# Kernel tuning notes

Measured on AMD Instinct MI355X. Metric: run time of the kernel, lower is better.

Reference implementation:

```python
import jax, jax.numpy as jnp
import numpy as np

B, N, M = 8, 131072, 64
M_VALID = 48  # trailing padding, matches remove_pad semantics
POSITIVE_IOU = 0.5
NEGATIVE_IOU = 0.3
CLASS_NUM = 1  # hardcoded in RpnTarget.__init__


def _make_boxes(key, shape_prefix, max_wh=64.0, span=1024.0):
    k1, k2, k3, k4 = jax.random.split(key, 4)
    x1 = jax.random.uniform(k1, shape_prefix, minval=0.0, maxval=span)
    y1 = jax.random.uniform(k2, shape_prefix, minval=0.0, maxval=span)
    w = jax.random.uniform(k3, shape_prefix, minval=4.0, maxval=max_wh)
    h = jax.random.uniform(k4, shape_prefix, minval=4.0, maxval=max_wh)
    return jnp.stack([x1, y1, x1 + w, y1 + h], axis=-1)


def setup_inputs() -> dict:
    key = jax.random.key(0)
    ka, kb = jax.random.split(key, 2)
    prior_anchors = _make_boxes(ka, (B, N))                       # [B,N,4]
    boxes = _make_boxes(kb, (B, M), max_wh=128.0)                 # [B,M,4]
    status = jnp.concatenate(
        [jnp.ones((B, M_VALID, 1)), jnp.zeros((B, M - M_VALID, 1))], axis=1
    )
    gt_bboxes = jnp.concatenate([boxes, status], axis=-1)          # [B,M,5]
    gt_class_idxes = jnp.zeros((B, M, 2), dtype=jnp.int32)         # zeroed in call()
    return {
        "prior_anchors": prior_anchors,
        "gt_bboxes": gt_bboxes,
        "gt_class_idxes": gt_class_idxes,
    }


def _bbox_transform(anchors, bboxes):
    # anchors, bboxes: [..., 4] in [x1,y1,x2,y2]
    ax = (anchors[..., 0] + anchors[..., 2]) * 0.5
    ay = (anchors[..., 1] + anchors[..., 3]) * 0.5
    aw = anchors[..., 2] - anchors[..., 0]
    ah = anchors[..., 3] - anchors[..., 1]
    bx = (bboxes[..., 0] + bboxes[..., 2]) * 0.5
    by = (bboxes[..., 1] + bboxes[..., 3]) * 0.5
    bw = bboxes[..., 2] - bboxes[..., 0]
    bh = bboxes[..., 3] - bboxes[..., 1]
    tx = (bx - ax) / aw
    ty = (by - ay) / ah
    tw = jnp.log(bw / aw)
    th = jnp.log(bh / ah)
    return jnp.stack([tx, ty, tw, th], axis=-1)


def _rpn_targets(prior_anchors, gt_bboxes, gt_class_idxes):
    boxes = gt_bboxes[..., :4]                 # [B,M,4]
    valid = gt_bboxes[..., 4] > 0              # [B,M] padding status

    a = prior_anchors[:, :, None, :]           # [B,N,1,4]
    b = boxes[:, None, :, :]                   # [B,1,M,4]
    inter_w = jnp.maximum(jnp.minimum(a[..., 2], b[..., 2]) - jnp.maximum(a[..., 0], b[..., 0]), 0.0)
    inter_h = jnp.maximum(jnp.minimum(a[..., 3], b[..., 3]) - jnp.maximum(a[..., 1], b[..., 1]), 0.0)
    inter = inter_w * inter_h                  # [B,N,M]
    area_a = jnp.maximum(a[..., 2] - a[..., 0], 0.0) * jnp.maximum(a[..., 3] - a[..., 1], 0.0)
    area_b = jnp.maximum(b[..., 2] - b[..., 0], 0.0) * jnp.maximum(b[..., 3] - b[..., 1], 0.0)
    iou = inter / (area_a + area_b - inter)    # [B,N,M]
    # mask out padded gt boxes (equivalent to remove_pad + trailing padding)
    iou = jnp.where(valid[:, None, :], iou, -1.0)

    max_iou = jnp.max(iou, axis=-1)            # [B,N]
    match_idx = jnp.argmax(iou, axis=-1)       # [B,N]
    positive = max_iou >= POSITIVE_IOU
    ignore = (max_iou >= NEGATIVE_IOU) & ~positive

    matched_boxes = jnp.take_along_axis(boxes, match_idx[..., None], axis=1)  # [B,N,4]
    reg = _bbox_transform(prior_anchors, matched_boxes)                        # [B,N,4]

    status = jnp.where(positive, 1.0, jnp.where(ignore, -1.0, 0.0))[..., None]  # [B,N,1]

    # call() zeros gt_class_idxes, so matched class idx is always 0; one_hot depth 1 -> ones
    cls_idx = jnp.take_along_axis(
        jnp.zeros_like(gt_class_idxes)[..., 0], match_idx, axis=1
    )                                                                           # [B,N] int32 zeros
    cls = jax.nn.one_hot(cls_idx, CLASS_NUM, dtype=reg.dtype)                   # [B,N,1]

    regression_targets = jnp.concatenate([reg, status], axis=-1)                # [B,N,5]
    classification_targets = jnp.concatenate([cls, status], axis=-1)            # [B,N,2]
    return regression_targets, classification_targets


def reference(prior_anchors, gt_bboxes, gt_class_idxes):
    return _rpn_targets(prior_anchors, gt_bboxes, gt_class_idxes)
```

## Files before the change

kernel.cpp:

```cpp
#include <hip/hip_runtime.h>


#define BB    8
#define NN    131072
#define MM    64
#define BLK   256
#define NBLK  (NN / BLK)
#define GC    16
#define CELLS (GC * GC)
#define CAP   32

#define WS_BOXES 0
#define WS_AREA  8192
#define WS_CNT   10240
#define WS_LIST  10272
#define WS_LEN   75808

typedef float  f4v __attribute__((ext_vector_type(4)));
typedef float  f2v __attribute__((ext_vector_type(2)));
typedef unsigned long long u64;
typedef unsigned char u8;

__global__ __launch_bounds__(256) void rpn_build_lists(
    const float* __restrict__ gt, char* __restrict__ ws)
{
    __shared__ float4 sbox[MM];
    __shared__ int    scnt;

    const int b = blockIdx.x;
    const int t = threadIdx.x;

    float4* wboxes = (float4*)(ws + WS_BOXES);
    float*  warea  = (float*)(ws + WS_AREA);
    int*    wcnt   = (int*)(ws + WS_CNT);
    u8*     wlist  = (u8*)(ws + WS_LIST);
    u8*     wlen   = (u8*)(ws + WS_LEN);

    if (t < MM) {
        const float* g = gt + ((size_t)b * MM + t) * 5;
        float x1 = g[0], y1 = g[1], x2 = g[2], y2 = g[3], st = g[4];
        bool valid = (st > 0.0f);
        u64 mask = __ballot(valid);
        int slot = __popcll(mask & ((1ull << t) - 1ull));
        int cntL = __popcll(mask);
        if (t == 0) { scnt = cntL; wcnt[b] = cntL; }
        if (valid) {
            float4 bx = make_float4(x1, y1, x2, y2);
            sbox[slot] = bx;
            wboxes[b * MM + slot] = bx;
            warea[b * MM + slot]  = fmaxf(x2 - x1, 0.0f) * fmaxf(y2 - y1, 0.0f);
        }
        if (t >= cntL) {
            wboxes[b * MM + t] = make_float4(0.f, 0.f, 0.f, 0.f);
            warea[b * MM + t]  = 0.f;
        }
    }
    __syncthreads();

    const int cnt = scnt;
    const int cx = t & (GC - 1), cy = t >> 4;
    const float wx1 = cx * 64.0f, wx2 = wx1 + 128.0f;
    const float wy1 = cy * 64.0f, wy2 = wy1 + 128.0f;

    u64* lq = (u64*)(wlist + ((size_t)b * CELLS + t) * CAP);
    lq[0] = ~0ull; lq[1] = ~0ull; lq[2] = ~0ull; lq[3] = ~0ull;
    u8* lst = (u8*)lq;

    int len = 0;
    for (int s = 0; s < cnt; ++s) {
        float4 bx = sbox[s];
        if (bx.x <= wx2 && bx.z >= wx1 && bx.y <= wy2 && bx.w >= wy1) {
            if (len < CAP) lst[len] = (u8)s;
            ++len;
        }
    }
    wlen[(size_t)b * CELLS + t] = (u8)len;
}

__global__ __launch_bounds__(BLK) void rpn_target_kernel(
    const float* __restrict__ anchors,
    const float* __restrict__ gt,
    const char* __restrict__ ws,
    float* __restrict__ out)
{
    constexpr float INV = GC / 1024.0f;

    __shared__ float sx1[MM], sy1[MM], sx2[MM], sy2[MM], sar[MM];
    __shared__ int   scnt;

    const int t = threadIdx.x;
    const int b = blockIdx.x / NBLK;
    const int n = (blockIdx.x % NBLK) * BLK + t;

    const f4v av = __builtin_nontemporal_load(
        (const f4v*)anchors + (size_t)b * NN + n);
    const float4 a = make_float4(av.x, av.y, av.z, av.w);

    if (t < MM) {
        float4 bx = ((const float4*)(ws + WS_BOXES))[b * MM + t];
        sx1[t] = bx.x; sy1[t] = bx.y; sx2[t] = bx.z; sy2[t] = bx.w;
        sar[t] = ((const float*)(ws + WS_AREA))[b * MM + t];
    }
    if (t == 0) scnt = ((const int*)(ws + WS_CNT))[b];

    int cx = (int)(a.x * INV); cx = cx < 0 ? 0 : (cx > GC - 1 ? GC - 1 : cx);
    int cy = (int)(a.y * INV); cy = cy < 0 ? 0 : (cy > GC - 1 ? GC - 1 : cy);
    const int cid = cy * GC + cx;

    const u64 lst8 = *(const u64*)(ws + WS_LIST + ((size_t)b * CELLS + cid) * CAP);
    const int len  = ((const u8*)(ws + WS_LEN))[(size_t)b * CELLS + cid];

    const float area_a = fmaxf(a.z - a.x, 0.0f) * fmaxf(a.w - a.y, 0.0f);

    __syncthreads();
    const int cnt = scnt;

    float best  = 0.0f;
    int   bslot = 0;

    float iou[8]; int id[8];
    #pragma unroll
    for (int j = 0; j < 8; ++j) {
        const int raw = (int)((lst8 >> (8 * j)) & 0xFFull);
        const int idx = raw & 63;
        id[j] = idx;
        const float bx1 = sx1[idx], by1 = sy1[idx];
        const float bx2 = sx2[idx], by2 = sy2[idx];
        float iw = fmaxf(fminf(a.z, bx2) - fmaxf(a.x, bx1), 0.0f);
        float ih = fmaxf(fminf(a.w, by2) - fmaxf(a.y, by1), 0.0f);
        float inter = iw * ih;
        inter = (raw != 255) ? inter : 0.0f;
        float denom = (area_a + sar[idx]) - inter;
        iou[j] = inter / denom;
    }
    #pragma unroll
    for (int j = 0; j < 8; ++j)
        if (iou[j] > best) { best = iou[j]; bslot = id[j]; }

    if (__any(len > 8)) {
        const u8* gl = (const u8*)(ws + WS_LIST + ((size_t)b * CELLS + cid) * CAP);
        const int L = (len <= CAP) ? len : 0;
        for (int j = 8; j < L; ++j) {
            const int idx = gl[j];
            float iw = fmaxf(fminf(a.z, sx2[idx]) - fmaxf(a.x, sx1[idx]), 0.0f);
            float ih = fmaxf(fminf(a.w, sy2[idx]) - fmaxf(a.y, sy1[idx]), 0.0f);
            float inter = iw * ih;
            if (inter > 0.0f) {
                float denom = (area_a + sar[idx]) - inter;
                float iou2 = inter / denom;
                if (iou2 > best) { best = iou2; bslot = idx; }
            }
        }
    }
    if (__any(len > CAP)) {
        if (len > CAP) {
            best = 0.0f; bslot = 0;
            for (int j = 0; j < cnt; ++j) {
                float iw = fmaxf(fminf(a.z, sx2[j]) - fmaxf(a.x, sx1[j]), 0.0f);
                float ih = fmaxf(fminf(a.w, sy2[j]) - fmaxf(a.y, sy1[j]), 0.0f);
                float inter = iw * ih;
                if (inter > 0.0f) {
                    float denom = (area_a + sar[j]) - inter;
                    float iou2 = inter / denom;
                    if (iou2 > best) { best = iou2; bslot = j; }
                }
            }
        }
    }

    const float status = (best >= 0.5f) ? 1.0f : ((best >= 0.3f) ? -1.0f : 0.0f);

    float mx1, my1, mx2, my2;
    if (cnt > 0) {
        mx1 = sx1[bslot]; my1 = sy1[bslot]; mx2 = sx2[bslot]; my2 = sy2[bslot];
    } else {
        const float* g0 = gt + (size_t)b * MM * 5;
        mx1 = g0[0]; my1 = g0[1]; mx2 = g0[2]; my2 = g0[3];
    }

    const float aw  = a.z - a.x;
    const float ah  = a.w - a.y;
    const float rw  = __builtin_amdgcn_rcpf(aw);
    const float rh  = __builtin_amdgcn_rcpf(ah);
    const float tx  = ((mx1 + mx2) * 0.5f - (a.x + a.z) * 0.5f) * rw;
    const float ty  = ((my1 + my2) * 0.5f - (a.y + a.w) * 0.5f) * rh;
    const float LN2 = 0.69314718055994531f;
    const float tw  = __builtin_amdgcn_logf((mx2 - mx1) * rw) * LN2;
    const float th  = __builtin_amdgcn_logf((my2 - my1) * rh) * LN2;

    const size_t gid = (size_t)b * NN + n;

    float* r = out + gid * 5;
    __builtin_nontemporal_store(tx,     &r[0]);
    __builtin_nontemporal_store(ty,     &r[1]);
    __builtin_nontemporal_store(tw,     &r[2]);
    __builtin_nontemporal_store(th,     &r[3]);
    __builtin_nontemporal_store(status, &r[4]);

    f2v cv; cv.x = 1.0f; cv.y = status;
    __builtin_nontemporal_store(cv, (f2v*)(out + (size_t)BB * NN * 5) + gid);
}

extern "C" void kernel_launch(void* const* d_in, const int* in_sizes, int n_in,
                              void* d_out, int out_size, void* d_ws, size_t ws_size,
                              hipStream_t stream) {
    const float* anchors = (const float*)d_in[0];
    const float* gt      = (const float*)d_in[1];

    float* out = (float*)d_out;
    char*  ws  = (char*)d_ws;

    hipLaunchKernelGGL(rpn_build_lists, dim3(BB), dim3(256), 0, stream, gt, ws);
    hipLaunchKernelGGL(rpn_target_kernel, dim3(BB * NBLK), dim3(BLK), 0, stream,
                       anchors, gt, ws, out);
}
```

Baseline: 25.60 us.

## Fuse list build and target kernels into one cooperative persistent kernel

Merges the grid-cell list construction and the per-anchor IoU/target kernel into a single cooperative launch. A grid-wide sync separates the two phases, and a persistent grid of 1024 blocks loops over the 4096 anchor slices. Nontemporal loads and stores are also replaced with ordinary ones. This removes one kernel launch and the gap between the two kernels, at the cost of grid-sync overhead, cooperative launch overhead, and reloading shared box data on every slice iteration.

```diff
diff --git a/kernel.cpp b/kernel.cpp
--- a/kernel.cpp
+++ b/kernel.cpp
@@ -1,4 +1,5 @@
 #include <hip/hip_runtime.h>
+#include <hip/hip_cooperative_groups.h>
 
 
 #define BB    8
@@ -6,6 +7,8 @@
 #define MM    64
 #define BLK   256
 #define NBLK  (NN / BLK)
+#define NSLICE (BB * NBLK)
+#define GRID  1024
 #define GC    16
 #define CELLS (GC * GC)
 #define CAP   32
@@ -16,189 +19,185 @@
 #define WS_LIST  10272
 #define WS_LEN   75808
 
-typedef float  f4v __attribute__((ext_vector_type(4)));
-typedef float  f2v __attribute__((ext_vector_type(2)));
 typedef unsigned long long u64;
 typedef unsigned char u8;
 
-__global__ __launch_bounds__(256) void rpn_build_lists(
-    const float* __restrict__ gt, char* __restrict__ ws)
-{
-    __shared__ float4 sbox[MM];
-    __shared__ int    scnt;
-
-    const int b = blockIdx.x;
-    const int t = threadIdx.x;
-
-    float4* wboxes = (float4*)(ws + WS_BOXES);
-    float*  warea  = (float*)(ws + WS_AREA);
-    int*    wcnt   = (int*)(ws + WS_CNT);
-    u8*     wlist  = (u8*)(ws + WS_LIST);
-    u8*     wlen   = (u8*)(ws + WS_LEN);
-
-    if (t < MM) {
-        const float* g = gt + ((size_t)b * MM + t) * 5;
-        float x1 = g[0], y1 = g[1], x2 = g[2], y2 = g[3], st = g[4];
-        bool valid = (st > 0.0f);
-        u64 mask = __ballot(valid);
-        int slot = __popcll(mask & ((1ull << t) - 1ull));
-        int cntL = __popcll(mask);
-        if (t == 0) { scnt = cntL; wcnt[b] = cntL; }
-        if (valid) {
-            float4 bx = make_float4(x1, y1, x2, y2);
-            sbox[slot] = bx;
-            wboxes[b * MM + slot] = bx;
-            warea[b * MM + slot]  = fmaxf(x2 - x1, 0.0f) * fmaxf(y2 - y1, 0.0f);
-        }
-        if (t >= cntL) {
-            wboxes[b * MM + t] = make_float4(0.f, 0.f, 0.f, 0.f);
-            warea[b * MM + t]  = 0.f;
-        }
-    }
-    __syncthreads();
-
-    const int cnt = scnt;
-    const int cx = t & (GC - 1), cy = t >> 4;
-    const float wx1 = cx * 64.0f, wx2 = wx1 + 128.0f;
-    const float wy1 = cy * 64.0f, wy2 = wy1 + 128.0f;
-
-    u64* lq = (u64*)(wlist + ((size_t)b * CELLS + t) * CAP);
-    lq[0] = ~0ull; lq[1] = ~0ull; lq[2] = ~0ull; lq[3] = ~0ull;
-    u8* lst = (u8*)lq;
-
-    int len = 0;
-    for (int s = 0; s < cnt; ++s) {
-        float4 bx = sbox[s];
-        if (bx.x <= wx2 && bx.z >= wx1 && bx.y <= wy2 && bx.w >= wy1) {
-            if (len < CAP) lst[len] = (u8)s;
-            ++len;
-        }
-    }
-    wlen[(size_t)b * CELLS + t] = (u8)len;
-}
-
-__global__ __launch_bounds__(BLK) void rpn_target_kernel(
+namespace cg = cooperative_groups;
+
+__global__ __launch_bounds__(BLK) void rpn_fused(
     const float* __restrict__ anchors,
     const float* __restrict__ gt,
-    const char* __restrict__ ws,
+    char* __restrict__ ws,
     float* __restrict__ out)
 {
     constexpr float INV = GC / 1024.0f;
 
-    __shared__ float sx1[MM], sy1[MM], sx2[MM], sy2[MM], sar[MM];
-    __shared__ int   scnt;
+    __shared__ float4 sbox[MM];
+    __shared__ float  sx1[MM], sy1[MM], sx2[MM], sy2[MM], sar[MM];
+    __shared__ int    scnt;
 
     const int t = threadIdx.x;
-    const int b = blockIdx.x / NBLK;
-    const int n = (blockIdx.x % NBLK) * BLK + t;
-
-    const f4v av = __builtin_nontemporal_load(
-        (const f4v*)anchors + (size_t)b * NN + n);
-    const float4 a = make_float4(av.x, av.y, av.z, av.w);
-
-    if (t < MM) {
-        float4 bx = ((const float4*)(ws + WS_BOXES))[b * MM + t];
-        sx1[t] = bx.x; sy1[t] = bx.y; sx2[t] = bx.z; sy2[t] = bx.w;
-        sar[t] = ((const float*)(ws + WS_AREA))[b * MM + t];
+
+    if (blockIdx.x < BB) {
+        const int b = blockIdx.x;
+
+        float4* wboxes = (float4*)(ws + WS_BOXES);
+        float*  warea  = (float*)(ws + WS_AREA);
+        int*    wcnt   = (int*)(ws + WS_CNT);
+        u8*     wlist  = (u8*)(ws + WS_LIST);
+        u8*     wlen   = (u8*)(ws + WS_LEN);
+
+        if (t < MM) {
+            const float* g = gt + ((size_t)b * MM + t) * 5;
+            float x1 = g[0], y1 = g[1], x2 = g[2], y2 = g[3], st = g[4];
+            bool valid = (st > 0.0f);
+            u64 mask = __ballot(valid);
+            int slot = __popcll(mask & ((1ull << t) - 1ull));
+            int cntL = __popcll(mask);
+            if (t == 0) { scnt = cntL; wcnt[b] = cntL; }
+            if (valid) {
+                float4 bx = make_float4(x1, y1, x2, y2);
+                sbox[slot] = bx;
+                wboxes[b * MM + slot] = bx;
+                warea[b * MM + slot]  = fmaxf(x2 - x1, 0.0f) * fmaxf(y2 - y1, 0.0f);
+            }
+            if (t >= cntL) {
+                wboxes[b * MM + t] = make_float4(0.f, 0.f, 0.f, 0.f);
+                warea[b * MM + t]  = 0.f;
+            }
+        }
+        __syncthreads();
+
+        const int cnt = scnt;
+        const int cx = t & (GC - 1), cy = t >> 4;
+        const float wx1 = cx * 64.0f, wx2 = wx1 + 128.0f;
+        const float wy1 = cy * 64.0f, wy2 = wy1 + 128.0f;
+
+        u64* lq = (u64*)(wlist + ((size_t)b * CELLS + t) * CAP);
+        lq[0] = ~0ull; lq[1] = ~0ull; lq[2] = ~0ull; lq[3] = ~0ull;
+        u8* lst = (u8*)lq;
+
+        int len = 0;
+        for (int s = 0; s < cnt; ++s) {
+            float4 bx = sbox[s];
+            if (bx.x <= wx2 && bx.z >= wx1 && bx.y <= wy2 && bx.w >= wy1) {
+                if (len < CAP) lst[len] = (u8)s;
+                ++len;
+            }
+        }
+        wlen[(size_t)b * CELLS + t] = (u8)len;
+        __threadfence();
     }
-    if (t == 0) scnt = ((const int*)(ws + WS_CNT))[b];
-
-    int cx = (int)(a.x * INV); cx = cx < 0 ? 0 : (cx > GC - 1 ? GC - 1 : cx);
-    int cy = (int)(a.y * INV); cy = cy < 0 ? 0 : (cy > GC - 1 ? GC - 1 : cy);
-    const int cid = cy * GC + cx;
-
-    const u64 lst8 = *(const u64*)(ws + WS_LIST + ((size_t)b * CELLS + cid) * CAP);
-    const int len  = ((const u8*)(ws + WS_LEN))[(size_t)b * CELLS + cid];
-
-    const float area_a = fmaxf(a.z - a.x, 0.0f) * fmaxf(a.w - a.y, 0.0f);
-
-    __syncthreads();
-    const int cnt = scnt;
-
-    float best  = 0.0f;
-    int   bslot = 0;
-
-    float iou[8]; int id[8];
-    #pragma unroll
-    for (int j = 0; j < 8; ++j) {
-        const int raw = (int)((lst8 >> (8 * j)) & 0xFFull);
-        const int idx = raw & 63;
-        id[j] = idx;
-        const float bx1 = sx1[idx], by1 = sy1[idx];
-        const float bx2 = sx2[idx], by2 = sy2[idx];
-        float iw = fmaxf(fminf(a.z, bx2) - fmaxf(a.x, bx1), 0.0f);
-        float ih = fmaxf(fminf(a.w, by2) - fmaxf(a.y, by1), 0.0f);
-        float inter = iw * ih;
-        inter = (raw != 255) ? inter : 0.0f;
-        float denom = (area_a + sar[idx]) - inter;
-        iou[j] = inter / denom;
-    }
-    #pragma unroll
-    for (int j = 0; j < 8; ++j)
-        if (iou[j] > best) { best = iou[j]; bslot = id[j]; }
-
-    if (__any(len > 8)) {
-        const u8* gl = (const u8*)(ws + WS_LIST + ((size_t)b * CELLS + cid) * CAP);
-        const int L = (len <= CAP) ? len : 0;
-        for (int j = 8; j < L; ++j) {
-            const int idx = gl[j];
-            float iw = fmaxf(fminf(a.z, sx2[idx]) - fmaxf(a.x, sx1[idx]), 0.0f);
-            float ih = fmaxf(fminf(a.w, sy2[idx]) - fmaxf(a.y, sy1[idx]), 0.0f);
+
+    cg::this_grid().sync();
+
+    for (int s = blockIdx.x; s < NSLICE; s += GRID) {
+        const int b = s / NBLK;
+        const int n = (s % NBLK) * BLK + t;
+
+        const float4 a = ((const float4*)anchors)[(size_t)b * NN + n];
+
+        __syncthreads();
+        if (t < MM) {
+            float4 bx = ((const float4*)(ws + WS_BOXES))[b * MM + t];
+            sx1[t] = bx.x; sy1[t] = bx.y; sx2[t] = bx.z; sy2[t] = bx.w;
+            sar[t] = ((const float*)(ws + WS_AREA))[b * MM + t];
+        }
+        if (t == 0) scnt = ((const int*)(ws + WS_CNT))[b];
+
+        int cx = (int)(a.x * INV); cx = cx < 0 ? 0 : (cx > GC - 1 ? GC - 1 : cx);
+        int cy = (int)(a.y * INV); cy = cy < 0 ? 0 : (cy > GC - 1 ? GC - 1 : cy);
+        const int cid = cy * GC + cx;
+
+        const u64 lst8 = *(const u64*)(ws + WS_LIST + ((size_t)b * CELLS + cid) * CAP);
+        const int len  = ((const u8*)(ws + WS_LEN))[(size_t)b * CELLS + cid];
+
+        const float area_a = fmaxf(a.z - a.x, 0.0f) * fmaxf(a.w - a.y, 0.0f);
+
+        __syncthreads();
+        const int cnt = scnt;
+
+        float best  = 0.0f;
+        int   bslot = 0;
+
+        float iou[8]; int id[8];
+        #pragma unroll
+        for (int j = 0; j < 8; ++j) {
+            const int raw = (int)((lst8 >> (8 * j)) & 0xFFull);
+            const int idx = raw & 63;
+            id[j] = idx;
+            const float bx1 = sx1[idx], by1 = sy1[idx];
+            const float bx2 = sx2[idx], by2 = sy2[idx];
+            float iw = fmaxf(fminf(a.z, bx2) - fmaxf(a.x, bx1), 0.0f);
+            float ih = fmaxf(fminf(a.w, by2) - fmaxf(a.y, by1), 0.0f);
             float inter = iw * ih;
-            if (inter > 0.0f) {
-                float denom = (area_a + sar[idx]) - inter;
-                float iou2 = inter / denom;
-                if (iou2 > best) { best = iou2; bslot = idx; }
-            }
-        }
-    }
-    if (__any(len > CAP)) {
-        if (len > CAP) {
-            best = 0.0f; bslot = 0;
-            for (int j = 0; j < cnt; ++j) {
-                float iw = fmaxf(fminf(a.z, sx2[j]) - fmaxf(a.x, sx1[j]), 0.0f);
-                float ih = fmaxf(fminf(a.w, sy2[j]) - fmaxf(a.y, sy1[j]), 0.0f);
+            inter = (raw != 255) ? inter : 0.0f;
+            float denom = (area_a + sar[idx]) - inter;
+            iou[j] = inter / denom;
+        }
+        #pragma unroll
+        for (int j = 0; j < 8; ++j)
+            if (iou[j] > best) { best = iou[j]; bslot = id[j]; }
+
+        if (__any(len > 8)) {
+            const u8* gl = (const u8*)(ws + WS_LIST + ((size_t)b * CELLS + cid) * CAP);
+            const int L = (len <= CAP) ? len : 0;
+            for (int j = 8; j < L; ++j) {
+                const int idx = gl[j];
+                float iw = fmaxf(fminf(a.z, sx2[idx]) - fmaxf(a.x, sx1[idx]), 0.0f);
+                float ih = fmaxf(fminf(a.w, sy2[idx]) - fmaxf(a.y, sy1[idx]), 0.0f);
                 float inter = iw * ih;
                 if (inter > 0.0f) {
-                    float denom = (area_a + sar[j]) - inter;
+                    float denom = (area_a + sar[idx]) - inter;
                     float iou2 = inter / denom;
-                    if (iou2 > best) { best = iou2; bslot = j; }
+                    if (iou2 > best) { best = iou2; bslot = idx; }
                 }
             }
         }
+        if (__any(len > CAP)) {
+            if (len > CAP) {
+                best = 0.0f; bslot = 0;
+                for (int j = 0; j < cnt; ++j) {
+                    float iw = fmaxf(fminf(a.z, sx2[j]) - fmaxf(a.x, sx1[j]), 0.0f);
+                    float ih = fmaxf(fminf(a.w, sy2[j]) - fmaxf(a.y, sy1[j]), 0.0f);
+                    float inter = iw * ih;
+                    if (inter > 0.0f) {
+                        float denom = (area_a + sar[j]) - inter;
+                        float iou2 = inter / denom;
+                        if (iou2 > best) { best = iou2; bslot = j; }
+                    }
+                }
+            }
+        }
+
+        const float status = (best >= 0.5f) ? 1.0f : ((best >= 0.3f) ? -1.0f : 0.0f);
+
+        float mx1, my1, mx2, my2;
+        if (cnt > 0) {
+            mx1 = sx1[bslot]; my1 = sy1[bslot]; mx2 = sx2[bslot]; my2 = sy2[bslot];
+        } else {
+            const float* g0 = gt + (size_t)b * MM * 5;
+            mx1 = g0[0]; my1 = g0[1]; mx2 = g0[2]; my2 = g0[3];
+        }
+
+        const float aw  = a.z - a.x;
+        const float ah  = a.w - a.y;
+        const float rw  = __builtin_amdgcn_rcpf(aw);
+        const float rh  = __builtin_amdgcn_rcpf(ah);
+        const float tx  = ((mx1 + mx2) * 0.5f - (a.x + a.z) * 0.5f) * rw;
+        const float ty  = ((my1 + my2) * 0.5f - (a.y + a.w) * 0.5f) * rh;
+        const float LN2 = 0.69314718055994531f;
+        const float tw  = __builtin_amdgcn_logf((mx2 - mx1) * rw) * LN2;
+        const float th  = __builtin_amdgcn_logf((my2 - my1) * rh) * LN2;
+
+        const size_t gid = (size_t)b * NN + n;
+
+        float* r = out + gid * 5;
+        r[0] = tx; r[1] = ty; r[2] = tw; r[3] = th; r[4] = status;
+
+        float2* c = (float2*)(out + (size_t)BB * NN * 5) + gid;
+        *c = make_float2(1.0f, status);
     }
-
-    const float status = (best >= 0.5f) ? 1.0f : ((best >= 0.3f) ? -1.0f : 0.0f);
-
-    float mx1, my1, mx2, my2;
-    if (cnt > 0) {
-        mx1 = sx1[bslot]; my1 = sy1[bslot]; mx2 = sx2[bslot]; my2 = sy2[bslot];
-    } else {
-        const float* g0 = gt + (size_t)b * MM * 5;
-        mx1 = g0[0]; my1 = g0[1]; mx2 = g0[2]; my2 = g0[3];
-    }
-
-    const float aw  = a.z - a.x;
-    const float ah  = a.w - a.y;
-    const float rw  = __builtin_amdgcn_rcpf(aw);
-    const float rh  = __builtin_amdgcn_rcpf(ah);
-    const float tx  = ((mx1 + mx2) * 0.5f - (a.x + a.z) * 0.5f) * rw;
-    const float ty  = ((my1 + my2) * 0.5f - (a.y + a.w) * 0.5f) * rh;
-    const float LN2 = 0.69314718055994531f;
-    const float tw  = __builtin_amdgcn_logf((mx2 - mx1) * rw) * LN2;
-    const float th  = __builtin_amdgcn_logf((my2 - my1) * rh) * LN2;
-
-    const size_t gid = (size_t)b * NN + n;
-
-    float* r = out + gid * 5;
-    __builtin_nontemporal_store(tx,     &r[0]);
-    __builtin_nontemporal_store(ty,     &r[1]);
-    __builtin_nontemporal_store(tw,     &r[2]);
-    __builtin_nontemporal_store(th,     &r[3]);
-    __builtin_nontemporal_store(status, &r[4]);
-
-    f2v cv; cv.x = 1.0f; cv.y = status;
-    __builtin_nontemporal_store(cv, (f2v*)(out + (size_t)BB * NN * 5) + gid);
 }
 
 extern "C" void kernel_launch(void* const* d_in, const int* in_sizes, int n_in,
@@ -210,7 +209,7 @@
     float* out = (float*)d_out;
     char*  ws  = (char*)d_ws;
 
-    hipLaunchKernelGGL(rpn_build_lists, dim3(BB), dim3(256), 0, stream, gt, ws);
-    hipLaunchKernelGGL(rpn_target_kernel, dim3(BB * NBLK), dim3(BLK), 0, stream,
-                       anchors, gt, ws, out);
+    void* args[] = { (void*)&anchors, (void*)&gt, (void*)&ws, (void*)&out };
+    hipLaunchCooperativeKernel((const void*)rpn_fused, dim3(GRID), dim3(BLK),
+                               args, 0, stream);
 }
```

After: 80.42 us. +214.1%, slower.
